# Optimization experiments

Hardware: AMD Instinct MI355X
Metric: run time of the kernel (lower is better)

## Reference

```python
import jax, jax.numpy as jnp
import numpy as np

B, S, D = 2, 2048, 2048
H, KVH = 32, 8
HD = D // H          # 64
Q_OUT = H * HD       # 2048
KV_OUT = KVH * HD    # 512
THETA = 10000.0


def setup_inputs() -> dict:
    key = jax.random.key(0)
    k1, k2, k3 = jax.random.split(key, 3)
    x = jax.random.normal(k1, (B, S, D), dtype=jnp.float32)
    w_qkv = jax.random.normal(k2, (Q_OUT + 2 * KV_OUT, D), dtype=jnp.float32) * 0.02
    w_out = jax.random.normal(k3, (D, D), dtype=jnp.float32) * 0.02
    gain = jnp.ones((1,), dtype=jnp.float32)
    return {"x": x, "w_qkv": w_qkv, "w_out": w_out, "gain": gain}


def _rope(t):
    # t: [b, s, h, hd]; non-interleaved (half-split) RoPE, positions = arange(s)
    s, hd = t.shape[1], t.shape[-1]
    inv_freq = 1.0 / (THETA ** (jnp.arange(0, hd // 2, dtype=jnp.float32) * 2.0 / hd))
    ang = jnp.arange(s, dtype=jnp.float32)[:, None] * inv_freq[None, :]  # [s, hd/2]
    cos = jnp.cos(ang)[None, :, None, :]
    sin = jnp.sin(ang)[None, :, None, :]
    t1, t2 = t[..., : hd // 2], t[..., hd // 2 :]
    return jnp.concatenate([t1 * cos - t2 * sin, t2 * cos + t1 * sin], axis=-1)


def _rmsnorm(t, eps=1e-6):
    # per-head-dim RMS normalization in fp32 (QK-norm)
    inv = jax.lax.rsqrt(jnp.mean(t * t, axis=-1, keepdims=True) + eps)
    return t * inv


def reference(x, w_qkv, w_out, gain):
    proj = jnp.einsum("bsd,od->bso", x, w_qkv)
    Q = proj[..., :Q_OUT].reshape(B, S, H, HD)
    K = proj[..., Q_OUT : Q_OUT + KV_OUT].reshape(B, S, KVH, HD)
    V = proj[..., Q_OUT + KV_OUT :].reshape(B, S, KVH, HD)

    Q = _rope(Q)
    K = _rope(K)

    # GQA: repeat_interleave kv heads to match query heads
    rep = H // KVH
    K = jnp.repeat(K, rep, axis=2)  # [b, s, H, hd]
    V = jnp.repeat(V, rep, axis=2)

    # value residual path (disabled): alpha1=1, alpha2=0, scale=1 -> V * rsqrt(1 + 1e-8)
    V = V * jax.lax.rsqrt(jnp.float32(1.0 + 1e-8))

    # QK-RMSNorm with learnable scalar gain on q
    Qn = _rmsnorm(Q) * gain
    Kn = _rmsnorm(K)

    scale = 1.0 / jnp.sqrt(jnp.float32(HD))
    scores = jnp.einsum("bqhd,bkhd->bhqk", Qn, Kn) * scale  # [b, H, S, S]
    causal = jnp.tril(jnp.ones((S, S), dtype=bool))
    scores = jnp.where(causal[None, None], scores, jnp.float32(-1e30))
    p = jax.nn.softmax(scores, axis=-1)
    attn = jnp.einsum("bhqk,bkhd->bqhd", p, V)  # [b, S, H, hd]

    # rearrange '(h b) seq hd -> b seq (h hd)': head index is outer in feature dim
    attn_cat = attn.transpose(0, 1, 2, 3).reshape(B, S, H * HD)
    attn_out = jnp.einsum("bsd,od->bso", attn_cat, w_out)

    # module returns (attn_out, V) with V in (h*b, seq, hd) layout
    V_flat = V.transpose(2, 0, 1, 3).reshape(H * B, S, HD)
    return attn_out, V_flat
```

## Files before the change

### kernel.cpp

```cpp
#include <hip/hip_runtime.h>
#include <hip/hip_bf16.h>
#include <cstdint>
#include <cstddef>

#define B_ 2
#define S_ 2048
#define D_ 2048
#define H_ 32
#define KVH_ 8
#define HD_ 64
#define PROJN 3072

typedef unsigned short u16;
typedef unsigned int u32;
typedef __attribute__((ext_vector_type(8))) short short8;
typedef __attribute__((ext_vector_type(4))) short short4v;
typedef __attribute__((ext_vector_type(4))) float f32x4;

__device__ __forceinline__ u16 f2bf(float f) {
  __hip_bfloat16 h = __float2bfloat16(f);
  return *reinterpret_cast<u16*>(&h);
}

__device__ __forceinline__ float fast_exp2(float x) {
  float r;
  asm("v_exp_f32 %0, %1" : "=v"(r) : "v"(x));
  return r;
}

__device__ __forceinline__ u32 pack2bf(float lo, float hi) {
  u32 a = __float_as_uint(lo) + 0x8000u;
  u32 b = __float_as_uint(hi) + 0x8000u;
  return __builtin_amdgcn_perm(b, a, 0x07060302);
}

#define GLDS16(g, l)                                                           \
  __builtin_amdgcn_global_load_lds(                                            \
      (const __attribute__((address_space(1))) void*)(g),                      \
      (__attribute__((address_space(3))) void*)(l), 16, 0, 0)

__global__ __launch_bounds__(256) void pack3(const float* __restrict__ x,
                                             const float* __restrict__ wqkv,
                                             const float* __restrict__ wout,
                                             u16* __restrict__ xb,
                                             u16* __restrict__ wqkvb,
                                             u16* __restrict__ woutb) {
  const int bid = blockIdx.x;
  const float* in;
  u16* out;
  int base;
  if (bid < 4096) { in = x; out = xb; base = bid; }
  else if (bid < 7168) { in = wqkv; out = wqkvb; base = bid - 4096; }
  else { in = wout; out = woutb; base = bid - 7168; }
  const int i = (base * 256 + threadIdx.x) * 8;
  const float4* p = reinterpret_cast<const float4*>(in + i);
  float4 a = p[0], b = p[1];
  union { short8 v; u16 u[8]; } r;
  r.u[0] = f2bf(a.x); r.u[1] = f2bf(a.y); r.u[2] = f2bf(a.z); r.u[3] = f2bf(a.w);
  r.u[4] = f2bf(b.x); r.u[5] = f2bf(b.y); r.u[6] = f2bf(b.z); r.u[7] = f2bf(b.w);
  *reinterpret_cast<short8*>(out + i) = r.v;
}

__global__ __launch_bounds__(256) void rope_tabT(float* __restrict__ tct,
                                                 float* __restrict__ tst) {
  int i = blockIdx.x * 256 + threadIdx.x;
  int j = i >> 11, s = i & 2047;
  float e = (float)(2 * j) / 64.0f;
  float inv_freq = 1.0f / powf(10000.0f, e);
  float ang = (float)s * inv_freq;
  tct[i] = cosf(ang);
  tst[i] = sinf(ang);
}

__global__ __launch_bounds__(512) void gemm_bt(const u16* __restrict__ A,
                                               const u16* __restrict__ Bw,
                                               float* __restrict__ C, int M,
                                               int N, int K) {
  __shared__ u16 As[2][128 * 64];
  __shared__ u16 Bs[2][128 * 64];
  const int tid = threadIdx.x;
  const int lane = tid & 63;
  const int wave = tid >> 6;
  const int ntile = N >> 7;
  const int m0 = (blockIdx.x / ntile) << 7;
  const int n0 = (blockIdx.x % ntile) << 7;
  const int wr = (wave >> 1) << 5;
  const int wc = (wave & 1) << 6;
  const int arow = lane & 15;
  const int kgrp = lane >> 4;

  const f32x4 zero4 = {0.f, 0.f, 0.f, 0.f};
  f32x4 acc[2][4];
#pragma unroll
  for (int m = 0; m < 2; m++)
#pragma unroll
    for (int n = 0; n < 4; n++) acc[m][n] = zero4;

  int srow[2], sslot[2];
#pragma unroll
  for (int i = 0; i < 2; i++) {
    int c = i * 512 + tid;
    srow[i] = c >> 3;
    sslot[i] = (c & 7) ^ (srow[i] & 7);
  }

  auto stage = [&](int kt, int buf) {
    const int k0 = kt << 6;
#pragma unroll
    for (int i = 0; i < 2; i++) {
      const u16* ga = A + (size_t)(m0 + srow[i]) * K + k0 + sslot[i] * 8;
      GLDS16(ga, As[buf] + (i * 512 + tid) * 8);
    }
#pragma unroll
    for (int i = 0; i < 2; i++) {
      const u16* gb = Bw + (size_t)(n0 + srow[i]) * K + k0 + sslot[i] * 8;
      GLDS16(gb, Bs[buf] + (i * 512 + tid) * 8);
    }
  };

  const int KT = K >> 6;
  stage(0, 0);
  stage(1, 1);
  int cur = 0;
  for (int kt = 0; kt < KT; kt++) {
    if (kt + 1 < KT) asm volatile("s_waitcnt vmcnt(4)" ::: "memory");
    else             asm volatile("s_waitcnt vmcnt(0)" ::: "memory");
    __builtin_amdgcn_s_barrier();
    __builtin_amdgcn_sched_barrier(0);
    const u16* Asb = As[cur];
    const u16* Bsb = Bs[cur];
#pragma unroll
    for (int ks = 0; ks < 2; ks++) {
      const int sd = ks * 4 + kgrp;
      short8 a[2], b[4];
#pragma unroll
      for (int m = 0; m < 2; m++) {
        int r = wr + m * 16 + arow;
        a[m] = *reinterpret_cast<const short8*>(Asb + r * 64 + ((sd ^ (r & 7)) << 3));
      }
#pragma unroll
      for (int n = 0; n < 4; n++) {
        int r = wc + n * 16 + arow;
        b[n] = *reinterpret_cast<const short8*>(Bsb + r * 64 + ((sd ^ (r & 7)) << 3));
      }
#pragma unroll
      for (int m = 0; m < 2; m++)
#pragma unroll
        for (int n = 0; n < 4; n++)
          acc[m][n] = __builtin_amdgcn_mfma_f32_16x16x32_bf16(a[m], b[n], acc[m][n], 0, 0, 0);
    }
    __builtin_amdgcn_sched_barrier(0);
    __builtin_amdgcn_s_barrier();
    if (kt + 2 < KT) stage(kt + 2, cur);
    cur ^= 1;
  }

  const int crow = kgrp * 4;
#pragma unroll
  for (int m = 0; m < 2; m++) {
#pragma unroll
    for (int n = 0; n < 4; n++) {
      float* cp = C + (size_t)(m0 + wr + m * 16 + crow) * N + n0 + wc + n * 16 + arow;
#pragma unroll
      for (int r = 0; r < 4; r++) cp[(size_t)r * N] = acc[m][n][r];
    }
  }
}

__global__ __launch_bounds__(512) void gemm_qkv(
    const u16* __restrict__ A, const u16* __restrict__ Bw,
    const float* __restrict__ tct, const float* __restrict__ tst,
    const float* __restrict__ gain, u16* __restrict__ Vt,
    float* __restrict__ Vout, u16* __restrict__ Qn, u16* __restrict__ Kn) {
  __shared__ u16 As[128 * 64];
  __shared__ u16 Bs[128 * 64];
  const int tid = threadIdx.x;
  const int lane = tid & 63;
  const int wave = tid >> 6;
  const int ntile = PROJN >> 7;
  const int m0 = (blockIdx.x / ntile) << 7;
  const int n0 = (blockIdx.x % ntile) << 7;
  const int wr = (wave >> 1) << 5;
  const int wc = (wave & 1) << 6;
  const int ql = lane & 15;
  const int g = lane >> 4;
  const int K = 2048;

  const f32x4 zero4 = {0.f, 0.f, 0.f, 0.f};
  f32x4 acc[2][4];
#pragma unroll
  for (int m = 0; m < 2; m++)
#pragma unroll
    for (int n = 0; n < 4; n++) acc[m][n] = zero4;

  int srow[2], sslot[2];
#pragma unroll
  for (int i = 0; i < 2; i++) {
    int c = i * 512 + tid;
    srow[i] = c >> 3;
    sslot[i] = (c & 7) ^ (srow[i] & 7);
  }

  auto stage = [&](int kt) {
    const int k0 = kt << 6;
#pragma unroll
    for (int i = 0; i < 2; i++) {
      const u16* ga = A + (size_t)(m0 + srow[i]) * K + k0 + sslot[i] * 8;
      GLDS16(ga, As + (i * 512 + tid) * 8);
    }
#pragma unroll
    for (int i = 0; i < 2; i++) {
      const u16* gb = Bw + (size_t)(n0 + srow[i]) * K + k0 + sslot[i] * 8;
      GLDS16(gb, Bs + (i * 512 + tid) * 8);
    }
  };

  stage(0);
  for (int kt = 0;; kt++) {
    __syncthreads();
#pragma unroll
    for (int ks = 0; ks < 2; ks++) {
      const int sd = ks * 4 + g;
      short8 a[2], b[4];
#pragma unroll
      for (int m = 0; m < 2; m++) {
        int r = wr + m * 16 + ql;
        a[m] = *reinterpret_cast<const short8*>(As + r * 64 + ((sd ^ (r & 7)) << 3));
      }
#pragma unroll
      for (int n = 0; n < 4; n++) {
        int r = wc + n * 16 + ql;
        b[n] = *reinterpret_cast<const short8*>(Bs + r * 64 + ((sd ^ (r & 7)) << 3));
      }
#pragma unroll
      for (int m = 0; m < 2; m++)
#pragma unroll
        for (int n = 0; n < 4; n++)
          acc[m][n] = __builtin_amdgcn_mfma_f32_16x16x32_bf16(a[m], b[n], acc[m][n], 0, 0, 0);
    }
    if (kt + 1 == 32) break;
    __syncthreads();
    stage(kt + 1);
  }

  const int hslice = (n0 + wc) >> 6;
  const int browbase = m0 + wr + 4 * g;

  if (hslice >= 40) {
    const int kvh2 = hslice - 40;
#pragma unroll
    for (int m = 0; m < 2; m++) {
      const int rowg = browbase + 16 * m;
      const int sb = rowg & (S_ - 1);
      const int bb2 = rowg >> 11;
#pragma unroll
      for (int n = 0; n < 4; n++) {
        const int d = n * 16 + ql;
        union { short4v v; u16 uu[4]; } pv;
#pragma unroll
        for (int r = 0; r < 4; r++) pv.uu[r] = f2bf(acc[m][n][r]);
        *reinterpret_cast<short4v*>(
            Vt + (((size_t)(bb2 * KVH_ + kvh2)) * HD_ + d) * S_ + sb) = pv.v;
#pragma unroll
        for (int hh = 0; hh < 4; hh++) {
          float* vd = Vout +
              (((size_t)((kvh2 * 4 + hh) * B_ + bb2)) * S_ + sb) * HD_ + d;
#pragma unroll
          for (int r = 0; r < 4; r++) vd[(size_t)r * HD_] = acc[m][n][r];
        }
      }
    }
    return;
  }

  const int bb = (m0 + wr) >> 11;
  const bool isQ = (hslice < 32);
  const float scale = isQ ? gain[0] * 0.18033688011112042f : 1.0f;
  u16* outp = isQ ? Qn + ((size_t)(bb * H_ + hslice)) * S_ * HD_
                  : Kn + ((size_t)(bb * KVH_ + (hslice - 32))) * S_ * HD_;
  const int jj0 = ql, jj1 = 16 + ql;

#pragma unroll
  for (int m = 0; m < 2; m++) {
    const int sb = (browbase + 16 * m) & (S_ - 1);
    float c0a[4], c1a[4], s0a[4], s1a[4];
    *reinterpret_cast<float4*>(c0a) = *reinterpret_cast<const float4*>(&tct[jj0 * 2048 + sb]);
    *reinterpret_cast<float4*>(c1a) = *reinterpret_cast<const float4*>(&tct[jj1 * 2048 + sb]);
    *reinterpret_cast<float4*>(s0a) = *reinterpret_cast<const float4*>(&tst[jj0 * 2048 + sb]);
    *reinterpret_cast<float4*>(s1a) = *reinterpret_cast<const float4*>(&tst[jj1 * 2048 + sb]);
    float o[4][4], iv[4];
#pragma unroll
    for (int r = 0; r < 4; r++) {
      const float a0 = acc[m][0][r], a1 = acc[m][1][r];
      const float a2 = acc[m][2][r], a3 = acc[m][3][r];
      const float l0 = a0 * c0a[r] - a2 * s0a[r];
      const float l1 = a1 * c1a[r] - a3 * s1a[r];
      const float h0 = a2 * c0a[r] + a0 * s0a[r];
      const float h1 = a3 * c1a[r] + a1 * s1a[r];
      o[0][r] = l0; o[1][r] = l1; o[2][r] = h0; o[3][r] = h1;
      float sr = (l0 * l0 + l1 * l1) + (h0 * h0 + h1 * h1);
      sr += __shfl_xor(sr, 1);
      sr += __shfl_xor(sr, 2);
      sr += __shfl_xor(sr, 4);
      sr += __shfl_xor(sr, 8);
      iv[r] = rsqrtf(sr * (1.0f / 64.0f) + 1e-6f) * scale;
    }
#pragma unroll
    for (int n = 0; n < 4; n++) {
      const int d = n * 16 + ql;
#pragma unroll
      for (int r = 0; r < 4; r++)
        outp[(size_t)(sb + r) * HD_ + d] = f2bf(o[n][r] * iv[r]);
    }
  }
}

__global__ __launch_bounds__(256, 2) void attn_fwd(const u16* __restrict__ Qn,
                                                   const u16* __restrict__ Kn,
                                                   const u16* __restrict__ Vt,
                                                   u16* __restrict__ Aout) {
  __shared__ u16 Ks[2][64 * 64];
  __shared__ u16 Vs[2][64 * 64];
  __shared__ u16 Ps[4][1024];
  const int bid = blockIdx.x;
  const int grp = bid & 15;
  const int i = bid >> 4;
  const int qt = 63 - i;
  const int b = grp >> 3;
  const int kvh = grp & 7;
  const int q0 = qt << 5;
  const int JT = (qt >> 1) + 1;
  const int tid = threadIdx.x;
  const int lane = tid & 63;
  const int wave = tid >> 6;
  const int h = kvh * 4 + wave;
  const int ql = lane & 15;
  const int g = lane >> 4;

  short8 qa[2][2];
  int rowq[2];
#pragma unroll
  for (int f = 0; f < 2; f++) {
    rowq[f] = q0 + 16 * f + ql;
    const u16* qb = Qn + (((size_t)(b * H_ + h)) * S_ + rowq[f]) * HD_;
    qa[f][0] = *reinterpret_cast<const short8*>(qb + g * 8);
    qa[f][1] = *reinterpret_cast<const short8*>(qb + 32 + g * 8);
  }

  const f32x4 zero4 = {0.f, 0.f, 0.f, 0.f};
  f32x4 oacc[4][2];
#pragma unroll
  for (int dn = 0; dn < 4; dn++)
#pragma unroll
    for (int f = 0; f < 2; f++) oacc[dn][f] = zero4;
  float psum[2] = {0.f, 0.f};

  const u16* kg = Kn + ((size_t)(b * KVH_ + kvh)) * S_ * HD_;
  const u16* vg = Vt + ((size_t)(b * KVH_ + kvh)) * HD_ * S_;

  const int c0 = tid, c1 = 256 + tid;
  const int r0 = c0 >> 3, sl0 = (c0 & 7) ^ (r0 & 7);
  const int r1 = c1 >> 3, sl1 = (c1 & 7) ^ (r1 & 7);
  const int xsw2 = (ql & 7) << 2;

  auto stage = [&](int jt, int buf) {
    const int j0 = jt << 6;
    GLDS16(kg + (size_t)(j0 + r0) * HD_ + sl0 * 8, Ks[buf] + c0 * 8);
    GLDS16(kg + (size_t)(j0 + r1) * HD_ + sl1 * 8, Ks[buf] + c1 * 8);
    GLDS16(vg + (size_t)r0 * S_ + j0 + sl0 * 8, Vs[buf] + c0 * 8);
    GLDS16(vg + (size_t)r1 * S_ + j0 + sl1 * 8, Vs[buf] + c1 * 8);
  };

  stage(0, 0);
  __syncthreads();
  int cur = 0;
  for (int jt = 0; jt < JT; jt++) {
    if (jt + 1 < JT) stage(jt + 1, cur ^ 1);
    const int j0 = jt << 6;
    const u16* ksb = Ks[cur];
    const u16* vsb = Vs[cur];
    const bool diag = (jt == JT - 1);

    f32x4 sc[4][2];
#pragma unroll
    for (int n = 0; n < 4; n++)
#pragma unroll
      for (int f = 0; f < 2; f++) sc[n][f] = zero4;
    __builtin_amdgcn_s_setprio(1);
#pragma unroll
    for (int ks = 0; ks < 2; ks++) {
      const int sd = ks * 4 + g;
#pragma unroll
      for (int n = 0; n < 4; n++) {
        const int r = n * 16 + ql;
        short8 kf = *reinterpret_cast<const short8*>(ksb + r * 64 + ((sd ^ (r & 7)) << 3));
        sc[n][0] = __builtin_amdgcn_mfma_f32_16x16x32_bf16(kf, qa[0][ks], sc[n][0], 0, 0, 0);
        sc[n][1] = __builtin_amdgcn_mfma_f32_16x16x32_bf16(kf, qa[1][ks], sc[n][1], 0, 0, 0);
      }
    }
    __builtin_amdgcn_s_setprio(0);

    short8 pa[2][2];
#pragma unroll
    for (int f = 0; f < 2; f++) {
      float pv[4][4];
#pragma unroll
      for (int n = 0; n < 4; n++)
#pragma unroll
        for (int r = 0; r < 4; r++)
          pv[n][r] = fast_exp2(sc[n][f][r]);
      if (diag) {
#pragma unroll
        for (int n = 0; n < 4; n++)
#pragma unroll
          for (int r = 0; r < 4; r++)
            if ((j0 + n * 16 + 4 * g + r) > rowq[f]) pv[n][r] = 0.f;
      }
      u32* pw32 = reinterpret_cast<u32*>(Ps[wave]);
#pragma unroll
      for (int n = 0; n < 4; n++) {
        psum[f] += (pv[n][0] + pv[n][1]) + (pv[n][2] + pv[n][3]);
        const int idx = ql * 32 + (((n << 3) + (g << 1)) ^ xsw2);
        pw32[idx] = pack2bf(pv[n][0], pv[n][1]);
        pw32[idx + 1] = pack2bf(pv[n][2], pv[n][3]);
      }
#pragma unroll
      for (int ks = 0; ks < 2; ks++)
        pa[f][ks] = *reinterpret_cast<const short8*>(
            Ps[wave] + ql * 64 + ((32 * ks + 8 * g) ^ (xsw2 << 1)));
    }

    __builtin_amdgcn_s_setprio(1);
#pragma unroll
    for (int ks = 0; ks < 2; ks++) {
      const int sd = ks * 4 + g;
#pragma unroll
      for (int dn = 0; dn < 4; dn++) {
        const int vr = dn * 16 + ql;
        short8 vf = *reinterpret_cast<const short8*>(vsb + vr * 64 + ((sd ^ (vr & 7)) << 3));
        oacc[dn][0] = __builtin_amdgcn_mfma_f32_16x16x32_bf16(vf, pa[0][ks], oacc[dn][0], 0, 0, 0);
        oacc[dn][1] = __builtin_amdgcn_mfma_f32_16x16x32_bf16(vf, pa[1][ks], oacc[dn][1], 0, 0, 0);
      }
    }
    __builtin_amdgcn_s_setprio(0);

    __syncthreads();
    cur ^= 1;
  }

#pragma unroll
  for (int f = 0; f < 2; f++) {
    float s = psum[f];
    s += __shfl_xor(s, 16);
    s += __shfl_xor(s, 32);
    const float il = 1.0f / s;
#pragma unroll
    for (int dn = 0; dn < 4; dn++) {
      union { short4v v; u16 uu[4]; } o;
#pragma unroll
      for (int r = 0; r < 4; r++) o.uu[r] = f2bf(oacc[dn][f][r] * il);
      u16* dst = Aout + ((size_t)b * S_ + rowq[f]) * D_ + h * HD_ + dn * 16 + 4 * g;
      *reinterpret_cast<short4v*>(dst) = o.v;
    }
  }
}

extern "C" void kernel_launch(void* const* d_in, const int* in_sizes, int n_in,
                              void* d_out, int out_size, void* d_ws,
                              size_t ws_size, hipStream_t stream) {
  const float* x = (const float*)d_in[0];
  const float* wqkv = (const float*)d_in[1];
  const float* wout = (const float*)d_in[2];
  const float* gain = (const float*)d_in[3];

  float* out_attn = (float*)d_out;
  float* out_vflat = out_attn + (size_t)B_ * S_ * D_;

  uint8_t* w = (uint8_t*)d_ws;
  u16* xb      = (u16*)(w);
  u16* wqkvb   = (u16*)(w + 16777216);
  u16* woutb   = (u16*)(w + 29360128);
  u16* Qn      = (u16*)(w + 37748736);
  u16* Kn      = (u16*)(w + 54525952);
  u16* Vt      = (u16*)(w + 58720256);
  u16* attnb   = (u16*)(w + 62914560);
  float* tct   = (float*)(w + 79691776);
  float* tst   = (float*)(w + 79953920);

  pack3<<<9216, 256, 0, stream>>>(x, wqkv, wout, xb, wqkvb, woutb);
  rope_tabT<<<256, 256, 0, stream>>>(tct, tst);

  gemm_qkv<<<(4096 / 128) * (3072 / 128), 512, 0, stream>>>(
      xb, wqkvb, tct, tst, gain, Vt, out_vflat, Qn, Kn);
  attn_fwd<<<B_ * KVH_ * (S_ / 32), 256, 0, stream>>>(Qn, Kn, Vt, attnb);
  gemm_bt<<<(4096 / 128) * (2048 / 128), 512, 0, stream>>>(attnb, woutb,
                                                           out_attn, 4096,
                                                           2048, 2048);
}
```

Measured before the change: 183.7 us.

## Widen attention q-tile to 64 rows with 8 waves; fold RoPE table into pack

The attention kernel now uses 512 threads, with two groups of four waves each covering a 32-row slice of a 64-row query tile. Each staged K/V tile is therefore reused by twice as many query rows, which halves global K/V traffic and the block count, and each thread stages one chunk instead of two. The diagonal tile is now 64x64, so masking must cover more of it, and the per-block causal imbalance changes. Separately, the RoPE table computation is merged into the pack kernel as extra blocks to save one launch.

```diff
diff --git a/kernel.cpp b/kernel.cpp
--- a/kernel.cpp
+++ b/kernel.cpp
@@ -44,8 +44,20 @@
                                              const float* __restrict__ wout,
                                              u16* __restrict__ xb,
                                              u16* __restrict__ wqkvb,
-                                             u16* __restrict__ woutb) {
+                                             u16* __restrict__ woutb,
+                                             float* __restrict__ tct,
+                                             float* __restrict__ tst) {
   const int bid = blockIdx.x;
+  if (bid >= 9216) {
+    int i = (bid - 9216) * 256 + threadIdx.x;
+    int j = i >> 11, s = i & 2047;
+    float e = (float)(2 * j) / 64.0f;
+    float inv_freq = 1.0f / powf(10000.0f, e);
+    float ang = (float)s * inv_freq;
+    tct[i] = cosf(ang);
+    tst[i] = sinf(ang);
+    return;
+  }
   const float* in;
   u16* out;
   int base;
@@ -59,17 +71,6 @@
   r.u[0] = f2bf(a.x); r.u[1] = f2bf(a.y); r.u[2] = f2bf(a.z); r.u[3] = f2bf(a.w);
   r.u[4] = f2bf(b.x); r.u[5] = f2bf(b.y); r.u[6] = f2bf(b.z); r.u[7] = f2bf(b.w);
   *reinterpret_cast<short8*>(out + i) = r.v;
-}
-
-__global__ __launch_bounds__(256) void rope_tabT(float* __restrict__ tct,
-                                                 float* __restrict__ tst) {
-  int i = blockIdx.x * 256 + threadIdx.x;
-  int j = i >> 11, s = i & 2047;
-  float e = (float)(2 * j) / 64.0f;
-  float inv_freq = 1.0f / powf(10000.0f, e);
-  float ang = (float)s * inv_freq;
-  tct[i] = cosf(ang);
-  tst[i] = sinf(ang);
 }
 
 __global__ __launch_bounds__(512) void gemm_bt(const u16* __restrict__ A,
@@ -315,25 +316,26 @@
   }
 }
 
-__global__ __launch_bounds__(256, 2) void attn_fwd(const u16* __restrict__ Qn,
-                                                   const u16* __restrict__ Kn,
-                                                   const u16* __restrict__ Vt,
-                                                   u16* __restrict__ Aout) {
+__global__ __launch_bounds__(512) void attn_fwd(const u16* __restrict__ Qn,
+                                                const u16* __restrict__ Kn,
+                                                const u16* __restrict__ Vt,
+                                                u16* __restrict__ Aout) {
   __shared__ u16 Ks[2][64 * 64];
   __shared__ u16 Vs[2][64 * 64];
-  __shared__ u16 Ps[4][1024];
+  __shared__ u16 Ps[8][1024];
   const int bid = blockIdx.x;
   const int grp = bid & 15;
   const int i = bid >> 4;
-  const int qt = 63 - i;
+  const int qt = 31 - i;
   const int b = grp >> 3;
   const int kvh = grp & 7;
-  const int q0 = qt << 5;
-  const int JT = (qt >> 1) + 1;
+  const int q0 = qt << 6;
+  const int JT = qt + 1;
   const int tid = threadIdx.x;
   const int lane = tid & 63;
   const int wave = tid >> 6;
-  const int h = kvh * 4 + wave;
+  const int h = kvh * 4 + (wave & 3);
+  const int sub = wave >> 2;
   const int ql = lane & 15;
   const int g = lane >> 4;
 
@@ -341,7 +343,7 @@
   int rowq[2];
 #pragma unroll
   for (int f = 0; f < 2; f++) {
-    rowq[f] = q0 + 16 * f + ql;
+    rowq[f] = q0 + 32 * sub + 16 * f + ql;
     const u16* qb = Qn + (((size_t)(b * H_ + h)) * S_ + rowq[f]) * HD_;
     qa[f][0] = *reinterpret_cast<const short8*>(qb + g * 8);
     qa[f][1] = *reinterpret_cast<const short8*>(qb + 32 + g * 8);
@@ -358,17 +360,13 @@
   const u16* kg = Kn + ((size_t)(b * KVH_ + kvh)) * S_ * HD_;
   const u16* vg = Vt + ((size_t)(b * KVH_ + kvh)) * HD_ * S_;
 
-  const int c0 = tid, c1 = 256 + tid;
-  const int r0 = c0 >> 3, sl0 = (c0 & 7) ^ (r0 & 7);
-  const int r1 = c1 >> 3, sl1 = (c1 & 7) ^ (r1 & 7);
+  const int r0 = tid >> 3, sl0 = (tid & 7) ^ (r0 & 7);
   const int xsw2 = (ql & 7) << 2;
 
   auto stage = [&](int jt, int buf) {
     const int j0 = jt << 6;
-    GLDS16(kg + (size_t)(j0 + r0) * HD_ + sl0 * 8, Ks[buf] + c0 * 8);
-    GLDS16(kg + (size_t)(j0 + r1) * HD_ + sl1 * 8, Ks[buf] + c1 * 8);
-    GLDS16(vg + (size_t)r0 * S_ + j0 + sl0 * 8, Vs[buf] + c0 * 8);
-    GLDS16(vg + (size_t)r1 * S_ + j0 + sl1 * 8, Vs[buf] + c1 * 8);
+    GLDS16(kg + (size_t)(j0 + r0) * HD_ + sl0 * 8, Ks[buf] + tid * 8);
+    GLDS16(vg + (size_t)r0 * S_ + j0 + sl0 * 8, Vs[buf] + tid * 8);
   };
 
   stage(0, 0);
@@ -487,12 +485,11 @@
   float* tct   = (float*)(w + 79691776);
   float* tst   = (float*)(w + 79953920);
 
-  pack3<<<9216, 256, 0, stream>>>(x, wqkv, wout, xb, wqkvb, woutb);
-  rope_tabT<<<256, 256, 0, stream>>>(tct, tst);
+  pack3<<<9472, 256, 0, stream>>>(x, wqkv, wout, xb, wqkvb, woutb, tct, tst);
 
   gemm_qkv<<<(4096 / 128) * (3072 / 128), 512, 0, stream>>>(
       xb, wqkvb, tct, tst, gain, Vt, out_vflat, Qn, Kn);
-  attn_fwd<<<B_ * KVH_ * (S_ / 32), 256, 0, stream>>>(Qn, Kn, Vt, attnb);
+  attn_fwd<<<B_ * KVH_ * (S_ / 64), 512, 0, stream>>>(Qn, Kn, Vt, attnb);
   gemm_bt<<<(4096 / 128) * (2048 / 128), 512, 0, stream>>>(attnb, woutb,
                                                            out_attn, 4096,
                                                            2048, 2048);
```

Measured after the change: 186.6 us. About the same (+1.6%).
